# Kernel tuning notes

Hardware: AMD Instinct MI355X
Metric: run time of the kernel (lower is better)

## Reference

```python
import jax, jax.numpy as jnp
import numpy as np

B, N, E, H = 2, 512, 128, 256
IN_DIM = 3 * E + 1


def setup_inputs() -> dict:
    key = jax.random.key(0)
    ks = jax.random.split(key, 9)
    node_embed = jax.random.normal(ks[0], (B, N, E), dtype=jnp.float32)
    problems = jax.random.uniform(ks[1], (B, N, 4), dtype=jnp.float32)
    euclid = jax.random.uniform(ks[2], (B, N, N), dtype=jnp.float32)
    euclid = 0.5 * (euclid + jnp.swapaxes(euclid, 1, 2))  # symmetric, realistic
    s = 0.02
    W1 = s * jax.random.normal(ks[3], (IN_DIM, H), dtype=jnp.float32)
    b1 = jnp.zeros((H,), jnp.float32)
    W2 = s * jax.random.normal(ks[4], (H, H), dtype=jnp.float32)
    b2 = jnp.zeros((H,), jnp.float32)
    W3 = s * jax.random.normal(ks[5], (H, 1), dtype=jnp.float32)
    b3 = jnp.zeros((1,), jnp.float32)
    return {"node_embed": node_embed, "problems": problems,
            "euclid_distance_matrix": euclid,
            "W1": W1, "b1": b1, "W2": W2, "b2": b2, "W3": W3, "b3": b3}


def _forward(node_embed, euclid, W1, b1, W2, b2, W3, b3):
    b, n, e = node_embed.shape
    hi = jnp.broadcast_to(node_embed[:, :, None, :], (b, n, n, e))
    hj = jnp.broadcast_to(node_embed[:, None, :, :], (b, n, n, e))
    habs = jnp.abs(node_embed[:, :, None, :] - node_embed[:, None, :, :])
    x = jnp.concatenate([hi, hj, habs, euclid[..., None]], axis=-1)  # (B,N,N,3E+1)
    h = jax.nn.relu(jnp.einsum('bijf,fh->bijh', x, W1) + b1)
    h = jax.nn.relu(jnp.einsum('bijh,hg->bijg', h, W2) + b2)
    pred = (jnp.einsum('bijh,ho->bijo', h, W3) + b3)[..., 0]  # (B,N,N)
    pred = 0.5 * (pred + jnp.swapaxes(pred, 1, 2))
    pred = pred * (1.0 - jnp.eye(n, dtype=pred.dtype))  # zero diagonal
    return pred


def reference(node_embed, problems, euclid_distance_matrix, W1, b1, W2, b2, W3, b3):
    # euclid_distance_matrix provided, so `problems` fallback path is unused
    return _forward(node_embed, euclid_distance_matrix, W1, b1, W2, b2, W3, b3)
```

## Files before the change

### kernel.cpp

```cpp
#include <hip/hip_runtime.h>
#include <hip/hip_bf16.h>


#define BN 512
#define EE 128
#define HH 256

typedef __attribute__((ext_vector_type(8)))  short short8;
typedef __attribute__((ext_vector_type(16))) float f32x16;
typedef __attribute__((ext_vector_type(4)))  float f32x4;

static __device__ __forceinline__ unsigned short f2bf(float f) {
    union { float f; unsigned u; } v; v.f = f;
    unsigned r = v.u + 0x7fff + ((v.u >> 16) & 1);
    return (unsigned short)(r >> 16);
}
static __device__ __forceinline__ float bf2f(unsigned short s) {
    union { unsigned u; float f; } v; v.u = ((unsigned)s) << 16;
    return v.f;
}
static __device__ __forceinline__ f32x16 zero16() {
    f32x16 v;
    #pragma unroll
    for (int i = 0; i < 16; ++i) v[i] = 0.f;
    return v;
}

__global__ void pack_weights(const float* __restrict__ W1, const float* __restrict__ W2,
                             unsigned short* __restrict__ w1c_p, unsigned short* __restrict__ w2_p) {
    int idx = blockIdx.x * 256 + threadIdx.x;
    if (idx < 32768) {
        int t = idx & 7, l = (idx >> 3) & 63, nb = (idx >> 9) & 7, kb = idx >> 12;
        int k = kb * 16 + (l >> 5) * 8 + t;
        int n = nb * 32 + (l & 31);
        w1c_p[idx] = f2bf(W1[(256 + k) * HH + n]);
    }
    if (idx < 65536) {
        int t = idx & 7, l = (idx >> 3) & 63, nb = (idx >> 9) & 7, kb = idx >> 12;
        int k = kb * 16 + (l >> 5) * 8 + t;
        int n = nb * 32 + (l & 31);
        w2_p[idx] = f2bf(W2[k * HH + n]);
    }
}

__global__ void precompute_pab(const float* __restrict__ node, const float* __restrict__ W1,
                               const float* __restrict__ b1,
                               float* __restrict__ PA, float* __restrict__ PB) {
    int bi = blockIdx.x;
    int h = threadIdx.x;
    const float* nd = node + (size_t)bi * EE;
    float sa = b1[h], sb = 0.f;
    #pragma unroll 4
    for (int e = 0; e < EE; ++e) {
        float x = nd[e];
        sa += x * W1[e * HH + h];
        sb += x * W1[(EE + e) * HH + h];
    }
    PA[bi * HH + h] = sa;
    PB[bi * HH + h] = sb;
}

__global__ __launch_bounds__(256, 3) void edge_main(
    const float* __restrict__ node, const float* __restrict__ euclid,
    const float* __restrict__ W1, const float* __restrict__ b2v,
    const float* __restrict__ W3, const float* __restrict__ b3,
    const float* __restrict__ PA, const float* __restrict__ PB,
    const unsigned short* __restrict__ w1c_p, const unsigned short* __restrict__ w2_p,
    float* __restrict__ out)
{
    __shared__ __align__(16) unsigned short lds_D[64 * 136];
    __shared__ __align__(16) unsigned short lds_h1[64 * 264];
    __shared__ float lds_e[64];

    const int jt = blockIdx.x, i = blockIdx.y, b = blockIdx.z;
    const int jbase = jt * 64;
    const int tid = threadIdx.x;
    const int wave = tid >> 6, lane = tid & 63;
    const int m0 = lane & 31, kq = (lane >> 5) * 8;

    float* hi_f = (float*)lds_h1;

    if (tid < 32)
        ((f32x4*)hi_f)[tid] = ((const f32x4*)(node + ((size_t)b * BN + i) * EE))[tid];
    if (tid < 64)
        lds_e[tid] = euclid[((size_t)b * BN + i) * BN + jbase + tid];
    __syncthreads();

    {
        int row = tid >> 2, q = tid & 3;
        const f32x4* nj = (const f32x4*)(node + ((size_t)b * BN + jbase + row) * EE);
        const f32x4* hv = (const f32x4*)hi_f;
        unsigned short* dst = &lds_D[row * 136 + q * 32];
        #pragma unroll
        for (int k = 0; k < 4; ++k) {
            f32x4 a0 = nj[q * 8 + k * 2 + 0];
            f32x4 h0 = hv[q * 8 + k * 2 + 0];
            f32x4 a1 = nj[q * 8 + k * 2 + 1];
            f32x4 h1 = hv[q * 8 + k * 2 + 1];
            short8 pk;
            #pragma unroll
            for (int u = 0; u < 4; ++u) {
                pk[u]     = (short)f2bf(fabsf(a0[u] - h0[u]));
                pk[4 + u] = (short)f2bf(fabsf(a1[u] - h1[u]));
            }
            *(short8*)(dst + k * 8) = pk;
        }
    }
    __syncthreads();

    f32x16 acc00 = zero16(), acc01 = zero16(), acc10 = zero16(), acc11 = zero16();
    {
        const short8* bp = (const short8*)w1c_p;
        #pragma unroll
        for (int kb = 0; kb < 8; ++kb) {
            short8 a0 = *(const short8*)&lds_D[m0 * 136 + kb * 16 + kq];
            short8 a1 = *(const short8*)&lds_D[(m0 + 32) * 136 + kb * 16 + kq];
            short8 b0 = bp[(kb * 8 + wave * 2 + 0) * 64 + lane];
            short8 b1 = bp[(kb * 8 + wave * 2 + 1) * 64 + lane];
            acc00 = __builtin_amdgcn_mfma_f32_32x32x16_bf16(a0, b0, acc00, 0, 0, 0);
            acc01 = __builtin_amdgcn_mfma_f32_32x32x16_bf16(a0, b1, acc01, 0, 0, 0);
            acc10 = __builtin_amdgcn_mfma_f32_32x32x16_bf16(a1, b0, acc10, 0, 0, 0);
            acc11 = __builtin_amdgcn_mfma_f32_32x32x16_bf16(a1, b1, acc11, 0, 0, 0);
        }
    }

    {
        const float* paRow  = PA + ((size_t)b * BN + i) * HH;
        const float* w1d    = W1 + 384 * HH;
        const float* pbBase = PB + ((size_t)b * BN + jbase) * HH;
        auto epi = [&](const f32x16& a, int mt, int nt) {
            int col = wave * 64 + nt * 32 + (lane & 31);
            float pac = paRow[col], wdc = w1d[col];
            #pragma unroll
            for (int r = 0; r < 16; ++r) {
                int row = mt * 32 + (r & 3) + 8 * (r >> 2) + 4 * (lane >> 5);
                float v = a[r] + pac + pbBase[row * HH + col] + lds_e[row] * wdc;
                v = v > 0.f ? v : 0.f;
                lds_h1[row * 264 + col] = f2bf(v);
            }
        };
        epi(acc00, 0, 0); epi(acc01, 0, 1); epi(acc10, 1, 0); epi(acc11, 1, 1);
    }
    __syncthreads();

    f32x16 c00 = zero16(), c01 = zero16(), c10 = zero16(), c11 = zero16();
    {
        const short8* bp = (const short8*)w2_p;
        #pragma unroll
        for (int kb = 0; kb < 16; ++kb) {
            short8 a0 = *(const short8*)&lds_h1[m0 * 264 + kb * 16 + kq];
            short8 a1 = *(const short8*)&lds_h1[(m0 + 32) * 264 + kb * 16 + kq];
            short8 b0 = bp[(kb * 8 + wave * 2 + 0) * 64 + lane];
            short8 b1 = bp[(kb * 8 + wave * 2 + 1) * 64 + lane];
            c00 = __builtin_amdgcn_mfma_f32_32x32x16_bf16(a0, b0, c00, 0, 0, 0);
            c01 = __builtin_amdgcn_mfma_f32_32x32x16_bf16(a0, b1, c01, 0, 0, 0);
            c10 = __builtin_amdgcn_mfma_f32_32x32x16_bf16(a1, b0, c10, 0, 0, 0);
            c11 = __builtin_amdgcn_mfma_f32_32x32x16_bf16(a1, b1, c11, 0, 0, 0);
        }
    }
    __syncthreads();

    {
        auto epi = [&](const f32x16& a, int mt, int nt) {
            int col = wave * 64 + nt * 32 + (lane & 31);
            float b2c = b2v[col];
            #pragma unroll
            for (int r = 0; r < 16; ++r) {
                int row = mt * 32 + (r & 3) + 8 * (r >> 2) + 4 * (lane >> 5);
                float v = a[r] + b2c;
                v = v > 0.f ? v : 0.f;
                lds_h1[row * 264 + col] = f2bf(v);
            }
        };
        epi(c00, 0, 0); epi(c01, 0, 1); epi(c10, 1, 0); epi(c11, 1, 1);
    }
    __syncthreads();

    {
        int r = tid & 63, part = tid >> 6;
        int c0 = part * 64;
        float s = 0.f;
        #pragma unroll
        for (int k = 0; k < 8; ++k) {
            short8 h8 = *(const short8*)&lds_h1[r * 264 + c0 + k * 8];
            #pragma unroll
            for (int u = 0; u < 8; ++u)
                s += bf2f((unsigned short)h8[u]) * W3[c0 + k * 8 + u];
        }
        ((float*)lds_D)[part * 64 + r] = s;
    }
    __syncthreads();
    if (tid < 64) {
        const float* pp = (const float*)lds_D;
        float v = pp[tid] + pp[64 + tid] + pp[128 + tid] + pp[192 + tid] + b3[0];
        out[((size_t)b * BN + i) * BN + jbase + tid] = v;
    }
}

__global__ void symmetrize(float* __restrict__ out) {
    int b = blockIdx.z, ti = blockIdx.y, tj = blockIdx.x;
    if (tj < ti) return;
    int i = ti * 32 + threadIdx.y, j = tj * 32 + threadIdx.x;
    float* p = out + (size_t)b * BN * BN;
    if (i == j) { p[(size_t)i * BN + j] = 0.f; return; }
    if (j < i) return;
    float a = p[(size_t)i * BN + j];
    float c = p[(size_t)j * BN + i];
    float v = 0.5f * (a + c);
    p[(size_t)i * BN + j] = v;
    p[(size_t)j * BN + i] = v;
}

extern "C" void kernel_launch(void* const* d_in, const int* in_sizes, int n_in,
                              void* d_out, int out_size, void* d_ws, size_t ws_size,
                              hipStream_t stream) {
    const float* node   = (const float*)d_in[0];
    const float* euclid = (const float*)d_in[2];
    const float* W1     = (const float*)d_in[3];
    const float* b1     = (const float*)d_in[4];
    const float* W2     = (const float*)d_in[5];
    const float* b2     = (const float*)d_in[6];
    const float* W3     = (const float*)d_in[7];
    const float* b3     = (const float*)d_in[8];
    float* out = (float*)d_out;

    char* ws = (char*)d_ws;
    float* PA = (float*)ws;
    float* PB = (float*)(ws + (1u << 20));
    unsigned short* w1c_p = (unsigned short*)(ws + (2u << 20));
    unsigned short* w2_p  = (unsigned short*)(ws + (2u << 20) + 65536);

    pack_weights<<<256, 256, 0, stream>>>(W1, W2, w1c_p, w2_p);
    precompute_pab<<<BN * 2, 256, 0, stream>>>(node, W1, b1, PA, PB);
    edge_main<<<dim3(BN / 64, BN, 2), 256, 0, stream>>>(
        node, euclid, W1, b2, W3, b3, PA, PB, w1c_p, w2_p, out);
    symmetrize<<<dim3(BN / 32, BN / 32, 2), dim3(32, 32), 0, stream>>>(out);
}
```

Measured before the change: 244.7 us.

## Fold PB, euclid and bias terms into MFMA accumulation instead of epilogue loads

The per-j projection of node_j through W1's second block is no longer precomputed in fp32 and loaded per element in the epilogue. It is computed inside the layer-1 MFMA loop from a pre-packed bf16 node tensor, and the euclid term and b2 bias are added via extra rank-1 MFMAs using packed weight rows. The layer-1 epilogue drops the large strided PB global reads, and LDS buffers are merged into one. In exchange layer 1 does twice the MFMA work, the PB and euclid contributions are now rounded to bf16, and the bf16 conversion helpers switch to compiler intrinsics.

```diff
diff --git a/kernel.cpp b/kernel.cpp
--- a/kernel.cpp
+++ b/kernel.cpp
@@ -11,13 +11,11 @@
 typedef __attribute__((ext_vector_type(4)))  float f32x4;
 
 static __device__ __forceinline__ unsigned short f2bf(float f) {
-    union { float f; unsigned u; } v; v.f = f;
-    unsigned r = v.u + 0x7fff + ((v.u >> 16) & 1);
-    return (unsigned short)(r >> 16);
+    __bf16 h = (__bf16)f;
+    return __builtin_bit_cast(unsigned short, h);
 }
 static __device__ __forceinline__ float bf2f(unsigned short s) {
-    union { unsigned u; float f; } v; v.u = ((unsigned)s) << 16;
-    return v.f;
+    return (float)__builtin_bit_cast(__bf16, s);
 }
 static __device__ __forceinline__ f32x16 zero16() {
     f32x16 v;
@@ -25,173 +23,200 @@
     for (int i = 0; i < 16; ++i) v[i] = 0.f;
     return v;
 }
-
-__global__ void pack_weights(const float* __restrict__ W1, const float* __restrict__ W2,
-                             unsigned short* __restrict__ w1c_p, unsigned short* __restrict__ w2_p) {
+#define MFMA(a, b, c) __builtin_amdgcn_mfma_f32_32x32x16_bf16((a), (b), (c), 0, 0, 0)
+
+__global__ void pack_all(const float* __restrict__ node, const float* __restrict__ W1,
+                         const float* __restrict__ W2, const float* __restrict__ b2,
+                         unsigned short* __restrict__ w1c_p, unsigned short* __restrict__ w1b_p,
+                         unsigned short* __restrict__ w2_p,  unsigned short* __restrict__ w1d_f,
+                         unsigned short* __restrict__ b2_f,  unsigned short* __restrict__ node_p) {
     int idx = blockIdx.x * 256 + threadIdx.x;
-    if (idx < 32768) {
-        int t = idx & 7, l = (idx >> 3) & 63, nb = (idx >> 9) & 7, kb = idx >> 12;
-        int k = kb * 16 + (l >> 5) * 8 + t;
-        int n = nb * 32 + (l & 31);
-        w1c_p[idx] = f2bf(W1[(256 + k) * HH + n]);
+    {
+        int t = idx & 7, l = (idx >> 3) & 63, kb = (idx >> 9) & 7;
+        int j32 = (idx >> 12) & 15, b = (idx >> 16) & 1;
+        int j = j32 * 32 + (l & 31), e = kb * 16 + (l >> 5) * 8 + t;
+        node_p[idx] = f2bf(node[((size_t)b * BN + j) * EE + e]);
     }
     if (idx < 65536) {
         int t = idx & 7, l = (idx >> 3) & 63, nb = (idx >> 9) & 7, kb = idx >> 12;
-        int k = kb * 16 + (l >> 5) * 8 + t;
+        int k = kb * 16 + (l >> 5) * 8 + t, n = nb * 32 + (l & 31);
+        w2_p[idx] = f2bf(W2[k * HH + n]);
+        if (idx < 32768) {
+            w1c_p[idx] = f2bf(W1[(2 * EE + k) * HH + n]);
+            w1b_p[idx] = f2bf(W1[(EE + k) * HH + n]);
+        }
+    }
+    if (idx < 4096) {
+        int t = idx & 7, l = (idx >> 3) & 63, nb = idx >> 9;
         int n = nb * 32 + (l & 31);
-        w2_p[idx] = f2bf(W2[k * HH + n]);
-    }
-}
-
-__global__ void precompute_pab(const float* __restrict__ node, const float* __restrict__ W1,
-                               const float* __restrict__ b1,
-                               float* __restrict__ PA, float* __restrict__ PB) {
-    int bi = blockIdx.x;
-    int h = threadIdx.x;
+        bool nz = (t == 0 && l < 32);
+        w1d_f[idx] = nz ? f2bf(W1[(3 * EE) * HH + n]) : (unsigned short)0;
+        b2_f[idx]  = nz ? f2bf(b2[n]) : (unsigned short)0;
+    }
+}
+
+__global__ void precompute_pa(const float* __restrict__ node, const float* __restrict__ W1,
+                              const float* __restrict__ b1, float* __restrict__ PA) {
+    int bi = blockIdx.x, h = threadIdx.x;
     const float* nd = node + (size_t)bi * EE;
-    float sa = b1[h], sb = 0.f;
-    #pragma unroll 4
-    for (int e = 0; e < EE; ++e) {
-        float x = nd[e];
-        sa += x * W1[e * HH + h];
-        sb += x * W1[(EE + e) * HH + h];
-    }
+    float sa = b1[h];
+    #pragma unroll 8
+    for (int e = 0; e < EE; ++e) sa += nd[e] * W1[e * HH + h];
     PA[bi * HH + h] = sa;
-    PB[bi * HH + h] = sb;
 }
 
 __global__ __launch_bounds__(256, 3) void edge_main(
     const float* __restrict__ node, const float* __restrict__ euclid,
-    const float* __restrict__ W1, const float* __restrict__ b2v,
     const float* __restrict__ W3, const float* __restrict__ b3,
-    const float* __restrict__ PA, const float* __restrict__ PB,
-    const unsigned short* __restrict__ w1c_p, const unsigned short* __restrict__ w2_p,
+    const float* __restrict__ PA,
+    const unsigned short* __restrict__ w1c_p, const unsigned short* __restrict__ w1b_p,
+    const unsigned short* __restrict__ w2_p,  const unsigned short* __restrict__ w1d_f,
+    const unsigned short* __restrict__ b2_f,  const unsigned short* __restrict__ node_p,
     float* __restrict__ out)
 {
-    __shared__ __align__(16) unsigned short lds_D[64 * 136];
-    __shared__ __align__(16) unsigned short lds_h1[64 * 264];
-    __shared__ float lds_e[64];
+    __shared__ __align__(16) unsigned short lds_buf[64 * 264];
+    __shared__ __align__(16) float hi_f[EE];
+    __shared__ float pp[256];
 
     const int jt = blockIdx.x, i = blockIdx.y, b = blockIdx.z;
     const int jbase = jt * 64;
-    const int tid = threadIdx.x;
-    const int wave = tid >> 6, lane = tid & 63;
+    const int tid = threadIdx.x, wave = tid >> 6, lane = tid & 63;
     const int m0 = lane & 31, kq = (lane >> 5) * 8;
-
-    float* hi_f = (float*)lds_h1;
 
     if (tid < 32)
         ((f32x4*)hi_f)[tid] = ((const f32x4*)(node + ((size_t)b * BN + i) * EE))[tid];
-    if (tid < 64)
-        lds_e[tid] = euclid[((size_t)b * BN + i) * BN + jbase + tid];
     __syncthreads();
 
     {
         int row = tid >> 2, q = tid & 3;
         const f32x4* nj = (const f32x4*)(node + ((size_t)b * BN + jbase + row) * EE);
         const f32x4* hv = (const f32x4*)hi_f;
-        unsigned short* dst = &lds_D[row * 136 + q * 32];
+        unsigned short* dst = &lds_buf[row * 136 + q * 32];
         #pragma unroll
         for (int k = 0; k < 4; ++k) {
-            f32x4 a0 = nj[q * 8 + k * 2 + 0];
-            f32x4 h0 = hv[q * 8 + k * 2 + 0];
-            f32x4 a1 = nj[q * 8 + k * 2 + 1];
-            f32x4 h1 = hv[q * 8 + k * 2 + 1];
+            f32x4 a0 = nj[q * 8 + k * 2 + 0], h0 = hv[q * 8 + k * 2 + 0];
+            f32x4 a1 = nj[q * 8 + k * 2 + 1], h1v = hv[q * 8 + k * 2 + 1];
             short8 pk;
             #pragma unroll
             for (int u = 0; u < 4; ++u) {
                 pk[u]     = (short)f2bf(fabsf(a0[u] - h0[u]));
-                pk[4 + u] = (short)f2bf(fabsf(a1[u] - h1[u]));
+                pk[4 + u] = (short)f2bf(fabsf(a1[u] - h1v[u]));
             }
             *(short8*)(dst + k * 8) = pk;
         }
     }
     __syncthreads();
 
-    f32x16 acc00 = zero16(), acc01 = zero16(), acc10 = zero16(), acc11 = zero16();
-    {
-        const short8* bp = (const short8*)w1c_p;
+    f32x16 a00 = zero16(), a01 = zero16(), a10 = zero16(), a11 = zero16();
+    {
+        const short8* bc = (const short8*)w1c_p;
+        const short8* bb = (const short8*)w1b_p;
+        const short8* np = (const short8*)node_p + (size_t)(b * 16 + jt * 2) * 8 * 64;
         #pragma unroll
         for (int kb = 0; kb < 8; ++kb) {
-            short8 a0 = *(const short8*)&lds_D[m0 * 136 + kb * 16 + kq];
-            short8 a1 = *(const short8*)&lds_D[(m0 + 32) * 136 + kb * 16 + kq];
+            short8 ad0 = *(const short8*)&lds_buf[m0 * 136 + kb * 16 + kq];
+            short8 ad1 = *(const short8*)&lds_buf[(m0 + 32) * 136 + kb * 16 + kq];
+            short8 ah0 = np[kb * 64 + lane];
+            short8 ah1 = np[(8 + kb) * 64 + lane];
+            short8 b0 = bc[(kb * 8 + wave * 2 + 0) * 64 + lane];
+            short8 b1 = bc[(kb * 8 + wave * 2 + 1) * 64 + lane];
+            short8 c0 = bb[(kb * 8 + wave * 2 + 0) * 64 + lane];
+            short8 c1 = bb[(kb * 8 + wave * 2 + 1) * 64 + lane];
+            a00 = MFMA(ad0, b0, a00); a01 = MFMA(ad0, b1, a01);
+            a10 = MFMA(ad1, b0, a10); a11 = MFMA(ad1, b1, a11);
+            a00 = MFMA(ah0, c0, a00); a01 = MFMA(ah0, c1, a01);
+            a10 = MFMA(ah1, c0, a10); a11 = MFMA(ah1, c1, a11);
+        }
+        const float* erow = euclid + ((size_t)b * BN + i) * BN + jbase;
+        short8 ae0, ae1;
+        #pragma unroll
+        for (int u = 0; u < 8; ++u) { ae0[u] = 0; ae1[u] = 0; }
+        if (lane < 32) {
+            ae0[0] = (short)f2bf(erow[m0]);
+            ae1[0] = (short)f2bf(erow[32 + m0]);
+        }
+        short8 d0 = ((const short8*)w1d_f)[(wave * 2 + 0) * 64 + lane];
+        short8 d1 = ((const short8*)w1d_f)[(wave * 2 + 1) * 64 + lane];
+        a00 = MFMA(ae0, d0, a00); a01 = MFMA(ae0, d1, a01);
+        a10 = MFMA(ae1, d0, a10); a11 = MFMA(ae1, d1, a11);
+    }
+    __syncthreads();
+
+    {
+        const float* paRow = PA + ((size_t)b * BN + i) * HH;
+        int col0 = wave * 64 + m0;
+        float pa0 = paRow[col0], pa1 = paRow[col0 + 32];
+        int rbase = 4 * (lane >> 5);
+        #pragma unroll
+        for (int r = 0; r < 16; ++r) {
+            int row = (r & 3) + 8 * (r >> 2) + rbase;
+            float v0 = a00[r] + pa0; v0 = v0 > 0.f ? v0 : 0.f;
+            float v1 = a01[r] + pa1; v1 = v1 > 0.f ? v1 : 0.f;
+            float v2 = a10[r] + pa0; v2 = v2 > 0.f ? v2 : 0.f;
+            float v3 = a11[r] + pa1; v3 = v3 > 0.f ? v3 : 0.f;
+            lds_buf[row * 264 + col0]             = f2bf(v0);
+            lds_buf[row * 264 + col0 + 32]        = f2bf(v1);
+            lds_buf[(row + 32) * 264 + col0]      = f2bf(v2);
+            lds_buf[(row + 32) * 264 + col0 + 32] = f2bf(v3);
+        }
+    }
+    __syncthreads();
+
+    f32x16 c00 = zero16(), c01 = zero16(), c10 = zero16(), c11 = zero16();
+    {
+        const short8* bp = (const short8*)w2_p;
+        #pragma unroll
+        for (int kb = 0; kb < 16; ++kb) {
+            short8 ad0 = *(const short8*)&lds_buf[m0 * 264 + kb * 16 + kq];
+            short8 ad1 = *(const short8*)&lds_buf[(m0 + 32) * 264 + kb * 16 + kq];
             short8 b0 = bp[(kb * 8 + wave * 2 + 0) * 64 + lane];
             short8 b1 = bp[(kb * 8 + wave * 2 + 1) * 64 + lane];
-            acc00 = __builtin_amdgcn_mfma_f32_32x32x16_bf16(a0, b0, acc00, 0, 0, 0);
-            acc01 = __builtin_amdgcn_mfma_f32_32x32x16_bf16(a0, b1, acc01, 0, 0, 0);
-            acc10 = __builtin_amdgcn_mfma_f32_32x32x16_bf16(a1, b0, acc10, 0, 0, 0);
-            acc11 = __builtin_amdgcn_mfma_f32_32x32x16_bf16(a1, b1, acc11, 0, 0, 0);
-        }
-    }
-
-    {
-        const float* paRow  = PA + ((size_t)b * BN + i) * HH;
-        const float* w1d    = W1 + 384 * HH;
-        const float* pbBase = PB + ((size_t)b * BN + jbase) * HH;
-        auto epi = [&](const f32x16& a, int mt, int nt) {
-            int col = wave * 64 + nt * 32 + (lane & 31);
-            float pac = paRow[col], wdc = w1d[col];
-            #pragma unroll
-            for (int r = 0; r < 16; ++r) {
-                int row = mt * 32 + (r & 3) + 8 * (r >> 2) + 4 * (lane >> 5);
-                float v = a[r] + pac + pbBase[row * HH + col] + lds_e[row] * wdc;
-                v = v > 0.f ? v : 0.f;
-                lds_h1[row * 264 + col] = f2bf(v);
-            }
-        };
-        epi(acc00, 0, 0); epi(acc01, 0, 1); epi(acc10, 1, 0); epi(acc11, 1, 1);
-    }
-    __syncthreads();
-
-    f32x16 c00 = zero16(), c01 = zero16(), c10 = zero16(), c11 = zero16();
-    {
-        const short8* bp = (const short8*)w2_p;
-        #pragma unroll
-        for (int kb = 0; kb < 16; ++kb) {
-            short8 a0 = *(const short8*)&lds_h1[m0 * 264 + kb * 16 + kq];
-            short8 a1 = *(const short8*)&lds_h1[(m0 + 32) * 264 + kb * 16 + kq];
-            short8 b0 = bp[(kb * 8 + wave * 2 + 0) * 64 + lane];
-            short8 b1 = bp[(kb * 8 + wave * 2 + 1) * 64 + lane];
-            c00 = __builtin_amdgcn_mfma_f32_32x32x16_bf16(a0, b0, c00, 0, 0, 0);
-            c01 = __builtin_amdgcn_mfma_f32_32x32x16_bf16(a0, b1, c01, 0, 0, 0);
-            c10 = __builtin_amdgcn_mfma_f32_32x32x16_bf16(a1, b0, c10, 0, 0, 0);
-            c11 = __builtin_amdgcn_mfma_f32_32x32x16_bf16(a1, b1, c11, 0, 0, 0);
-        }
-    }
-    __syncthreads();
-
-    {
-        auto epi = [&](const f32x16& a, int mt, int nt) {
-            int col = wave * 64 + nt * 32 + (lane & 31);
-            float b2c = b2v[col];
-            #pragma unroll
-            for (int r = 0; r < 16; ++r) {
-                int row = mt * 32 + (r & 3) + 8 * (r >> 2) + 4 * (lane >> 5);
-                float v = a[r] + b2c;
-                v = v > 0.f ? v : 0.f;
-                lds_h1[row * 264 + col] = f2bf(v);
-            }
-        };
-        epi(c00, 0, 0); epi(c01, 0, 1); epi(c10, 1, 0); epi(c11, 1, 1);
-    }
-    __syncthreads();
-
-    {
-        int r = tid & 63, part = tid >> 6;
-        int c0 = part * 64;
+            c00 = MFMA(ad0, b0, c00); c01 = MFMA(ad0, b1, c01);
+            c10 = MFMA(ad1, b0, c10); c11 = MFMA(ad1, b1, c11);
+        }
+        short8 aone;
+        #pragma unroll
+        for (int u = 0; u < 8; ++u) aone[u] = 0;
+        if (lane < 32) aone[0] = (short)0x3F80;
+        short8 e0 = ((const short8*)b2_f)[(wave * 2 + 0) * 64 + lane];
+        short8 e1 = ((const short8*)b2_f)[(wave * 2 + 1) * 64 + lane];
+        c00 = MFMA(aone, e0, c00); c01 = MFMA(aone, e1, c01);
+        c10 = MFMA(aone, e0, c10); c11 = MFMA(aone, e1, c11);
+    }
+    __syncthreads();
+
+    {
+        int col0 = wave * 64 + m0;
+        int rbase = 4 * (lane >> 5);
+        #pragma unroll
+        for (int r = 0; r < 16; ++r) {
+            int row = (r & 3) + 8 * (r >> 2) + rbase;
+            float v0 = c00[r] > 0.f ? c00[r] : 0.f;
+            float v1 = c01[r] > 0.f ? c01[r] : 0.f;
+            float v2 = c10[r] > 0.f ? c10[r] : 0.f;
+            float v3 = c11[r] > 0.f ? c11[r] : 0.f;
+            lds_buf[row * 264 + col0]             = f2bf(v0);
+            lds_buf[row * 264 + col0 + 32]        = f2bf(v1);
+            lds_buf[(row + 32) * 264 + col0]      = f2bf(v2);
+            lds_buf[(row + 32) * 264 + col0 + 32] = f2bf(v3);
+        }
+    }
+    __syncthreads();
+
+    {
+        int r = tid & 63, part = tid >> 6, c0 = part * 64;
         float s = 0.f;
         #pragma unroll
         for (int k = 0; k < 8; ++k) {
-            short8 h8 = *(const short8*)&lds_h1[r * 264 + c0 + k * 8];
+            short8 h8 = *(const short8*)&lds_buf[r * 264 + c0 + k * 8];
             #pragma unroll
             for (int u = 0; u < 8; ++u)
                 s += bf2f((unsigned short)h8[u]) * W3[c0 + k * 8 + u];
         }
-        ((float*)lds_D)[part * 64 + r] = s;
+        pp[part * 64 + r] = s;
     }
     __syncthreads();
     if (tid < 64) {
-        const float* pp = (const float*)lds_D;
         float v = pp[tid] + pp[64 + tid] + pp[128 + tid] + pp[192 + tid] + b3[0];
         out[((size_t)b * BN + i) * BN + jbase + tid] = v;
     }
@@ -225,14 +250,17 @@
     float* out = (float*)d_out;
 
     char* ws = (char*)d_ws;
-    float* PA = (float*)ws;
-    float* PB = (float*)(ws + (1u << 20));
-    unsigned short* w1c_p = (unsigned short*)(ws + (2u << 20));
-    unsigned short* w2_p  = (unsigned short*)(ws + (2u << 20) + 65536);
-
-    pack_weights<<<256, 256, 0, stream>>>(W1, W2, w1c_p, w2_p);
-    precompute_pab<<<BN * 2, 256, 0, stream>>>(node, W1, b1, PA, PB);
+    float*          PA     = (float*)ws;
+    unsigned short* w1c_p  = (unsigned short*)(ws + (1u << 20));
+    unsigned short* w1b_p  = (unsigned short*)(ws + (1u << 20) + 65536);
+    unsigned short* w2_p   = (unsigned short*)(ws + (1u << 20) + 131072);
+    unsigned short* w1d_f  = (unsigned short*)(ws + (1u << 20) + 262144);
+    unsigned short* b2_f   = (unsigned short*)(ws + (1u << 20) + 270336);
+    unsigned short* node_p = (unsigned short*)(ws + (1u << 20) + 278528);
+
+    pack_all<<<512, 256, 0, stream>>>(node, W1, W2, b2, w1c_p, w1b_p, w2_p, w1d_f, b2_f, node_p);
+    precompute_pa<<<BN * 2, 256, 0, stream>>>(node, W1, b1, PA);
     edge_main<<<dim3(BN / 64, BN, 2), 256, 0, stream>>>(
-        node, euclid, W1, b2, W3, b3, PA, PB, w1c_p, w2_p, out);
+        node, euclid, W3, b3, PA, w1c_p, w1b_p, w2_p, w1d_f, b2_f, node_p, out);
     symmetrize<<<dim3(BN / 32, BN / 32, 2), dim3(32, 32), 0, stream>>>(out);
 }
```

Result: slower. 255.5 us (+4.4%).
